# Performance work log

Hardware: AMD Instinct MI355X
Metric: run time of the kernel (lower is better)

Reference implementation:

```python
import jax, jax.numpy as jnp
import numpy as np

N = 100000   # nodes
E = 800000   # edges
F = 64       # num_features == hidden_dim
D = 64       # hidden_dim
L = 3        # num_gc_layers
NG = 512     # num graphs in batch
BN_EPS = 1e-5


def setup_inputs() -> dict:
    key = jax.random.key(0)
    ks = jax.random.split(key, 16)
    s = 0.05
    return {
        "x": jax.random.normal(ks[0], (N, F), jnp.float32),
        "edge_index": jax.random.randint(ks[1], (2, E), 0, N),
        "batch": jnp.sort(jax.random.randint(ks[2], (N,), 0, NG)),
        "W1": jax.random.normal(ks[3], (L, F, D), jnp.float32) * s,
        "b1": jnp.zeros((L, D), jnp.float32),
        "W2": jax.random.normal(ks[4], (L, D, D), jnp.float32) * s,
        "b2": jnp.zeros((L, D), jnp.float32),
        "gin_eps": jnp.zeros((L,), jnp.float32),
        "gin_bias": jnp.zeros((L, D), jnp.float32),
        "bn_gamma": jnp.ones((L, D), jnp.float32),
        "bn_beta": jnp.zeros((L, D), jnp.float32),
        "Wp1": jax.random.normal(ks[5], (L * D, L * D), jnp.float32) * s,
        "bp1": jnp.zeros((L * D,), jnp.float32),
        "Wp2": jax.random.normal(ks[6], (L * D, L * D), jnp.float32) * s,
        "bp2": jnp.zeros((L * D,), jnp.float32),
    }


def reference(x, edge_index, batch, W1, b1, W2, b2, gin_eps, gin_bias,
              bn_gamma, bn_beta, Wp1, bp1, Wp2, bp2):
    row, col = edge_index[0], edge_index[1]
    h = x
    xs = []
    for i in range(L):
        # sparse adj @ h : sum over incoming edges (adj[row, col] = 1)
        agg = jax.ops.segment_sum(h[col], row, num_segments=N)
        z = (1.0 + gin_eps[i]) * h + agg
        # GIN internal MLP: Linear -> ReLU -> Linear -> ReLU
        z = jax.nn.relu(z @ W1[i] + b1[i])
        z = jax.nn.relu(z @ W2[i] + b2[i])
        # conv bias + relu (outer F.relu in Encoder is idempotent)
        z = jax.nn.relu(z + gin_bias[i])
        # BatchNorm1d, training mode: batch stats over nodes, biased variance
        mean = jnp.mean(z, axis=0)
        var = jnp.mean(jnp.square(z - mean), axis=0)
        h = (z - mean) * jax.lax.rsqrt(var + BN_EPS) * bn_gamma[i] + bn_beta[i]
        xs.append(h)
    # per-layer global add pool over graphs, then concat -> [NG, L*D]
    pooled = jnp.concatenate(
        [jax.ops.segment_sum(xi, batch, num_segments=NG) for xi in xs], axis=1)
    # projection head: Linear -> ReLU -> Linear
    y = jax.nn.relu(pooled @ Wp1 + bp1) @ Wp2 + bp2
    return y
```

## Files before the change

kernel.cpp:

```cpp
#include <hip/hip_runtime.h>

#define N_NODES 100000
#define N_EDGES 800000
#define DF 64
#define NGRAPH 512
#define LDIM 192
#define BN_EPS 1e-5
#define NTILES 6250
#define GIN_GRID 782
#define NWT (GIN_GRID * 8)
#define COLS_CAP 2600000
#define NBUCK 782
#define BCAP 2048
#define NBLK 128
#define CHUNK 6250
#define REGION_CAP 6144
#define PROJ_ROWS 8

typedef __attribute__((ext_vector_type(8))) short bf16x8;
typedef __attribute__((ext_vector_type(4))) float f32x4;

__device__ inline short f2bf(float x) {
    union { float f; unsigned u; } v; v.f = x;
    unsigned r = v.u + 0x7fff + ((v.u >> 16) & 1);
    return (short)(r >> 16);
}
__device__ inline float bf2f(unsigned short u) {
    union { unsigned u; float f; } v; v.u = ((unsigned)u) << 16; return v.f;
}
__device__ inline float bflo(unsigned u) {
    union { unsigned x; float f; } v; v.x = u << 16; return v.f;
}
__device__ inline float bfhi(unsigned u) {
    union { unsigned x; float f; } v; v.x = u & 0xffff0000u; return v.f;
}

__global__ __launch_bounds__(256) void x2bf_kernel(
    const float* __restrict__ x, unsigned short* __restrict__ xb)
{
    int i = blockIdx.x * 256 + threadIdx.x;
    const int total = N_NODES * DF / 8;
    if (i >= total) return;
    const float4* src = (const float4*)(x + (size_t)i * 8);
    float4 a = src[0], b = src[1];
    unsigned short u0 = (unsigned short)f2bf(a.x), u1 = (unsigned short)f2bf(a.y);
    unsigned short u2 = (unsigned short)f2bf(a.z), u3 = (unsigned short)f2bf(a.w);
    unsigned short u4 = (unsigned short)f2bf(b.x), u5 = (unsigned short)f2bf(b.y);
    unsigned short u6 = (unsigned short)f2bf(b.z), u7 = (unsigned short)f2bf(b.w);
    uint4 o;
    o.x = (unsigned)u0 | ((unsigned)u1 << 16);
    o.y = (unsigned)u2 | ((unsigned)u3 << 16);
    o.z = (unsigned)u4 | ((unsigned)u5 << 16);
    o.w = (unsigned)u6 | ((unsigned)u7 << 16);
    ((uint4*)xb)[i] = o;
}

__global__ __launch_bounds__(256) void blk_hist_kernel(
    const int* __restrict__ ei, int* __restrict__ hist)
{
    __shared__ int hh[NBUCK];
    int blk = blockIdx.x, tid = threadIdx.x;
    for (int i = tid; i < NBUCK; i += 256) hh[i] = 0;
    __syncthreads();
    int start = blk * CHUNK, end = min(start + CHUNK, N_EDGES);
    for (int e = start + tid; e < end; e += 256)
        atomicAdd(&hh[ei[e] >> 7], 1);
    __syncthreads();
    for (int i = tid; i < NBUCK; i += 256) hist[blk * NBUCK + i] = hh[i];
}

__global__ __launch_bounds__(NBLK) void blk_scan_kernel(
    const int* __restrict__ hist, int* __restrict__ pos, int* __restrict__ cnt)
{
    __shared__ int buf[NBLK];
    int k = blockIdx.x, b = threadIdx.x;
    int v = hist[b * NBUCK + k];
    buf[b] = v;
    __syncthreads();
    for (int o = 1; o < NBLK; o <<= 1) {
        int t = (b >= o) ? buf[b - o] : 0;
        __syncthreads();
        buf[b] += t;
        __syncthreads();
    }
    pos[b * NBUCK + k] = buf[b] - v;
    if (b == NBLK - 1) cnt[k] = buf[b];
}

__global__ __launch_bounds__(256) void place_kernel(
    const int* __restrict__ ei, const int* __restrict__ pos,
    unsigned* __restrict__ bucketData)
{
    __shared__ int cursor[NBUCK];
    int blk = blockIdx.x, tid = threadIdx.x;
    for (int i = tid; i < NBUCK; i += 256) cursor[i] = pos[blk * NBUCK + i];
    __syncthreads();
    int start = blk * CHUNK, end = min(start + CHUNK, N_EDGES);
    for (int e = start + tid; e < end; e += 256) {
        int r = ei[e];
        int c = ei[N_EDGES + e];
        int k = r >> 7;
        int p = atomicAdd(&cursor[k], 1);
        bucketData[(size_t)k * BCAP + p] = ((unsigned)(r & 127) << 17) | (unsigned)c;
    }
}

__global__ __launch_bounds__(256) void bucket_count_kernel(
    const unsigned* __restrict__ bucketData, const int* __restrict__ cnt,
    int* __restrict__ deg, int* __restrict__ bpad)
{
    __shared__ int rc[128];
    __shared__ int wps[16];
    int b = blockIdx.x, tid = threadIdx.x;
    int rowbase = b << 7;
    int nrows = min(128, N_NODES - rowbase);
    int cntb = cnt[b];
    if (tid < 128) rc[tid] = 0;
    __syncthreads();
    for (int e = tid; e < cntb; e += 256)
        atomicAdd(&rc[bucketData[(size_t)b * BCAP + e] >> 17], 1);
    __syncthreads();
    if (tid < nrows) deg[rowbase + tid] = rc[tid];
    if (tid < 16) {
        int m = 0;
        #pragma unroll
        for (int i = 0; i < 8; ++i) m = max(m, rc[tid * 8 + i]);
        wps[tid] = (m + 1) & ~1;
    }
    __syncthreads();
    if (tid == 0) {
        int s = 0;
        #pragma unroll
        for (int pk = 0; pk < 16; ++pk) s += 8 * wps[pk];
        bpad[b] = s;
    }
}

__global__ __launch_bounds__(1024) void bucket_scan_kernel(
    const int* __restrict__ bpad, int* __restrict__ bbase)
{
    __shared__ int buf[1024];
    int tid = threadIdx.x;
    int own = (tid < NBUCK) ? bpad[tid] : 0;
    buf[tid] = own;
    __syncthreads();
    for (int o = 1; o < 1024; o <<= 1) {
        int t = (tid >= o) ? buf[tid - o] : 0;
        __syncthreads();
        buf[tid] += t;
        __syncthreads();
    }
    if (tid < NBUCK) bbase[tid] = buf[tid] - own;
}

__global__ __launch_bounds__(256) void bucket_emit_kernel(
    const unsigned* __restrict__ bucketData, const int* __restrict__ cnt,
    const int* __restrict__ bbase,
    int* __restrict__ colT, int* __restrict__ offT, int* __restrict__ widT)
{
    __shared__ int rc[128], rcur[128];
    __shared__ int wps[16], pstart[16];
    __shared__ int region[REGION_CAP];
    __shared__ int totalS;
    int b = blockIdx.x, tid = threadIdx.x;
    int rowbase = b << 7;
    int nrows = min(128, N_NODES - rowbase);
    int cntb = cnt[b];
    int base = bbase[b];
    if (tid < 128) { rc[tid] = 0; rcur[tid] = 0; }
    __syncthreads();
    for (int e = tid; e < cntb; e += 256)
        atomicAdd(&rc[bucketData[(size_t)b * BCAP + e] >> 17], 1);
    __syncthreads();
    if (tid < 16) {
        int m = 0;
        #pragma unroll
        for (int i = 0; i < 8; ++i) m = max(m, rc[tid * 8 + i]);
        wps[tid] = (m + 1) & ~1;
    }
    __syncthreads();
    if (tid == 0) {
        int run = 0;
        #pragma unroll
        for (int pk = 0; pk < 16; ++pk) { pstart[pk] = run; run += 8 * wps[pk]; }
        totalS = run;
    }
    __syncthreads();
    int total = totalS;
    for (int e = tid; e < cntb; e += 256) {
        unsigned p = bucketData[(size_t)b * BCAP + e];
        int lr = p >> 17;
        int c = p & 0x1FFFF;
        int slot = atomicAdd(&rcur[lr], 1);
        int pk = lr >> 3, g = lr & 7;
        region[pstart[pk] + slot * 8 + g] = c * DF;
    }
    __syncthreads();
    for (int i = tid; i < nrows; i += 256) {
        int pk = i >> 3, g = i & 7;
        int wp = wps[pk];
        int sent = (rowbase + i) * DF;
        for (int slot = rc[i]; slot < wp; ++slot)
            region[pstart[pk] + slot * 8 + g] = sent;
    }
    __syncthreads();
    for (int k = tid; k < total; k += 256) colT[base + k] = region[k];
    if (tid < 16 && tid * 8 < nrows) {
        offT[b * 16 + tid] = base + pstart[tid];
        widT[b * 16 + tid] = wps[tid];
    }
}

__global__ __launch_bounds__(256) void gstart_kernel(
    const int* __restrict__ batch, int* __restrict__ gstart,
    float* __restrict__ idsc, float* __restrict__ idsh)
{
    int g = blockIdx.x * 256 + threadIdx.x;
    if (g < 64) { idsc[g] = 1.0f; idsh[g] = 0.0f; }
    if (g > NGRAPH) return;
    if (g == NGRAPH) { gstart[g] = N_NODES; return; }
    int lo = 0, hi = N_NODES;
    while (lo < hi) {
        int mid = (lo + hi) >> 1;
        if (batch[mid] < g) lo = mid + 1; else hi = mid;
    }
    gstart[g] = lo;
}

__global__ __launch_bounds__(256) void pack_w_kernel(
    const float* __restrict__ W1, const float* __restrict__ W2,
    short* __restrict__ Wpk)
{
    int u = blockIdx.x;
    int layer = u >> 1, gm = u & 1;
    const float* W = (gm ? W2 : W1) + layer * 4096;
    short* dst = Wpk + u * 4096;
    for (int idx = threadIdx.x; idx < 4096; idx += 256) {
        int i = idx & 7;
        int l = (idx >> 3) & 63;
        int rest = idx >> 9;
        int kt = rest & 1, nt = rest >> 1;
        int k = kt * 32 + (l >> 4) * 8 + i;
        int n = nt * 16 + (l & 15);
        dst[idx] = f2bf(W[k * 64 + n]);
    }
}

__global__ __launch_bounds__(512) void gin_layer_kernel(
    const unsigned short* __restrict__ zpb,
    const float* __restrict__ sc_in,
    const float* __restrict__ sh_in,
    const int* __restrict__ offT,
    const int* __restrict__ widT,
    const int* __restrict__ deg,
    const int* __restrict__ colT,
    const int* __restrict__ batch,
    unsigned short* __restrict__ zout,
    float* __restrict__ pooled,
    int lOff,
    const short* __restrict__ Wpk,
    const float* __restrict__ b1,
    const float* __restrict__ b2,
    const float* __restrict__ gin_eps,
    const float* __restrict__ gin_bias,
    float* __restrict__ part_s,
    float* __restrict__ part_q)
{
    __shared__ __align__(16) short Wp1s[4096];
    __shared__ __align__(16) short Wp2s[4096];
    __shared__ __align__(16) short zs[8][16 * 80];

    int tid = threadIdx.x;
    {
        const short4* s1 = (const short4*)Wpk;
        const short4* s2 = (const short4*)(Wpk + 4096);
        short4* d1 = (short4*)Wp1s;
        short4* d2 = (short4*)Wp2s;
        for (int i = tid; i < 1024; i += 512) { d1[i] = s1[i]; d2[i] = s2[i]; }
    }

    int w = tid >> 6, l = tid & 63;
    int lr = l & 15;
    int lk = l >> 4;
    int g8 = l >> 3;
    int j8 = l & 7;
    float epsf = 1.0f + gin_eps[0];
    float b1f[4], b2f[4], gbf[4];
    #pragma unroll
    for (int nt = 0; nt < 4; ++nt) {
        b1f[nt] = b1[nt * 16 + lr];
        b2f[nt] = b2[nt * 16 + lr];
        gbf[nt] = gin_bias[nt * 16 + lr];
    }
    float4 sca = *(const float4*)&sc_in[j8 * 8];
    float4 scb = *(const float4*)&sc_in[j8 * 8 + 4];
    float4 sha = *(const float4*)&sh_in[j8 * 8];
    float4 shb = *(const float4*)&sh_in[j8 * 8 + 4];
    float ssum[4] = {0, 0, 0, 0}, sq[4] = {0, 0, 0, 0};
    short* zw = zs[w];
    __syncthreads();

    int t = blockIdx.x * 8 + w;
    bool active = t < NTILES;
    int n0 = t * 16;
    int g0 = 0;
    bool uni = true;
    int gr[4];

    if (active) {
        g0 = batch[n0];
        int gl = batch[n0 + (l & 15)];
        uni = __all(gl == g0);
        if (!uni) {
            #pragma unroll
            for (int r = 0; r < 4; ++r) gr[r] = batch[n0 + lk * 4 + r];
        }

        #pragma unroll
        for (int half = 0; half < 2; ++half) {
            int p = t * 2 + half;
            int nP0 = p * 8;
            int sP = __builtin_amdgcn_readfirstlane(offT[p]);
            int wP = __builtin_amdgcn_readfirstlane(widT[p]);
            float acc[8];
            #pragma unroll
            for (int i = 0; i < 8; ++i) acc[i] = 0.0f;
            if (wP > 0) {
                int co0 = colT[sP + g8];
                int co1 = colT[sP + 8 + g8];
                uint4 v0 = *(const uint4*)(zpb + co0 + j8 * 8);
                uint4 v1 = *(const uint4*)(zpb + co1 + j8 * 8);
                #pragma unroll 1
                for (int it = 2; it < wP; it += 2) {
                    int cn0 = colT[sP + it * 8 + g8];
                    int cn1 = colT[sP + it * 8 + 8 + g8];
                    uint4 nv0 = *(const uint4*)(zpb + cn0 + j8 * 8);
                    uint4 nv1 = *(const uint4*)(zpb + cn1 + j8 * 8);
                    acc[0] += bflo(v0.x) + bflo(v1.x);
                    acc[1] += bfhi(v0.x) + bfhi(v1.x);
                    acc[2] += bflo(v0.y) + bflo(v1.y);
                    acc[3] += bfhi(v0.y) + bfhi(v1.y);
                    acc[4] += bflo(v0.z) + bflo(v1.z);
                    acc[5] += bfhi(v0.z) + bfhi(v1.z);
                    acc[6] += bflo(v0.w) + bflo(v1.w);
                    acc[7] += bfhi(v0.w) + bfhi(v1.w);
                    v0 = nv0; v1 = nv1;
                }
                acc[0] += bflo(v0.x) + bflo(v1.x);
                acc[1] += bfhi(v0.x) + bfhi(v1.x);
                acc[2] += bflo(v0.y) + bflo(v1.y);
                acc[3] += bfhi(v0.y) + bfhi(v1.y);
                acc[4] += bflo(v0.z) + bflo(v1.z);
                acc[5] += bfhi(v0.z) + bfhi(v1.z);
                acc[6] += bflo(v0.w) + bflo(v1.w);
                acc[7] += bfhi(v0.w) + bfhi(v1.w);
            }
            int node = nP0 + g8;
            int d = deg[node];
            uint4 hv = *(const uint4*)(zpb + node * DF + j8 * 8);
            float hn[8] = { bflo(hv.x), bfhi(hv.x), bflo(hv.y), bfhi(hv.y),
                            bflo(hv.z), bfhi(hv.z), bflo(hv.w), bfhi(hv.w) };
            float np = (float)(wP - d);
            float em = epsf - np;
            float dh = epsf + (float)d;
            float scv[8] = { sca.x, sca.y, sca.z, sca.w, scb.x, scb.y, scb.z, scb.w };
            float shv[8] = { sha.x, sha.y, sha.z, sha.w, shb.x, shb.y, shb.z, shb.w };
            unsigned short us[8];
            #pragma unroll
            for (int i = 0; i < 8; ++i) {
                float zf = scv[i] * (em * hn[i] + acc[i]) + dh * shv[i];
                us[i] = (unsigned short)f2bf(zf);
            }
            uint4 zpk;
            zpk.x = (unsigned)us[0] | ((unsigned)us[1] << 16);
            zpk.y = (unsigned)us[2] | ((unsigned)us[3] << 16);
            zpk.z = (unsigned)us[4] | ((unsigned)us[5] << 16);
            zpk.w = (unsigned)us[6] | ((unsigned)us[7] << 16);
            *(uint4*)&zw[(half * 8 + g8) * 80 + j8 * 8] = zpk;
        }

        {
            bf16x8 a0 = *(const bf16x8*)&zw[lr * 80 + lk * 8];
            bf16x8 a1 = *(const bf16x8*)&zw[lr * 80 + 32 + lk * 8];
            #pragma unroll
            for (int nt = 0; nt < 4; ++nt) {
                f32x4 acc = {0.f, 0.f, 0.f, 0.f};
                bf16x8 bb0 = *(const bf16x8*)&Wp1s[((nt * 2 + 0) * 64 + l) * 8];
                bf16x8 bb1 = *(const bf16x8*)&Wp1s[((nt * 2 + 1) * 64 + l) * 8];
                acc = __builtin_amdgcn_mfma_f32_16x16x32_bf16(a0, bb0, acc, 0, 0, 0);
                acc = __builtin_amdgcn_mfma_f32_16x16x32_bf16(a1, bb1, acc, 0, 0, 0);
                #pragma unroll
                for (int r = 0; r < 4; ++r) {
                    float v = fmaxf(acc[r] + b1f[nt], 0.0f);
                    zw[(lk * 4 + r) * 80 + nt * 16 + lr] = f2bf(v);
                }
            }
        }

        {
            bf16x8 a0 = *(const bf16x8*)&zw[lr * 80 + lk * 8];
            bf16x8 a1 = *(const bf16x8*)&zw[lr * 80 + 32 + lk * 8];
            #pragma unroll
            for (int nt = 0; nt < 4; ++nt) {
                f32x4 acc = {0.f, 0.f, 0.f, 0.f};
                bf16x8 bb0 = *(const bf16x8*)&Wp2s[((nt * 2 + 0) * 64 + l) * 8];
                bf16x8 bb1 = *(const bf16x8*)&Wp2s[((nt * 2 + 1) * 64 + l) * 8];
                acc = __builtin_amdgcn_mfma_f32_16x16x32_bf16(a0, bb0, acc, 0, 0, 0);
                acc = __builtin_amdgcn_mfma_f32_16x16x32_bf16(a1, bb1, acc, 0, 0, 0);
                #pragma unroll
                for (int r = 0; r < 4; ++r) {
                    float v = fmaxf(fmaxf(acc[r] + b2f[nt], 0.0f) + gbf[nt], 0.0f);
                    unsigned short vb = (unsigned short)f2bf(v);
                    zout[(n0 + lk * 4 + r) * DF + nt * 16 + lr] = vb;
                    float vr = bf2f(vb);
                    ssum[nt] += vr;
                    sq[nt] += vr * vr;
                    if (!uni)
                        unsafeAtomicAdd(&pooled[gr[r] * LDIM + lOff + nt * 16 + lr], vr);
                }
            }
        }
    }

    float svv[4];
    #pragma unroll
    for (int nt = 0; nt < 4; ++nt) {
        float sv = ssum[nt], qv = sq[nt];
        sv += __shfl_xor(sv, 16, 64); sv += __shfl_xor(sv, 32, 64);
        qv += __shfl_xor(qv, 16, 64); qv += __shfl_xor(qv, 32, 64);
        svv[nt] = sv;
        if (l < 16) {
            part_s[(nt * 16 + l) * NWT + t] = sv;
            part_q[(nt * 16 + l) * NWT + t] = qv;
        }
    }
    if (active && uni && l < 16) {
        #pragma unroll
        for (int nt = 0; nt < 4; ++nt)
            unsafeAtomicAdd(&pooled[g0 * LDIM + lOff + nt * 16 + l], svv[nt]);
    }
}

__global__ __launch_bounds__(256) void stat_reduce_kernel(
    const float* __restrict__ part_s, const float* __restrict__ part_q,
    const float* __restrict__ gamma, const float* __restrict__ beta,
    float* __restrict__ scale, float* __restrict__ shift)
{
    __shared__ double rs[4], rq[4];
    int f = blockIdx.x, tid = threadIdx.x;
    double s = 0.0, q = 0.0;
    for (int j = tid; j < NWT; j += 256) {
        s += (double)part_s[f * NWT + j];
        q += (double)part_q[f * NWT + j];
    }
    for (int o = 32; o > 0; o >>= 1) {
        s += __shfl_down(s, o, 64);
        q += __shfl_down(q, o, 64);
    }
    if ((tid & 63) == 0) { rs[tid >> 6] = s; rq[tid >> 6] = q; }
    __syncthreads();
    if (tid == 0) {
        double st = rs[0] + rs[1] + rs[2] + rs[3];
        double qt = rq[0] + rq[1] + rq[2] + rq[3];
        double mean = st / N_NODES;
        double var = qt / N_NODES - mean * mean;
        double inv = (double)gamma[f] / sqrt(var + BN_EPS);
        scale[f] = (float)inv;
        shift[f] = (float)((double)beta[f] - mean * inv);
    }
}

__global__ __launch_bounds__(192) void proj_fused_kernel(
    const float* __restrict__ praw,
    const float* __restrict__ scale3, const float* __restrict__ shift3,
    const int* __restrict__ gstart,
    const float* __restrict__ Wp1, const float* __restrict__ bp1,
    const float* __restrict__ Wp2, const float* __restrict__ bp2,
    float* __restrict__ out)
{
    __shared__ float rowS[PROJ_ROWS][LDIM];
    __shared__ float hid[PROJ_ROWS][LDIM];
    int r0 = blockIdx.x * PROJ_ROWS;
    int c = threadIdx.x;
    float scc = scale3[c], shc = shift3[c];
    #pragma unroll
    for (int r = 0; r < PROJ_ROWS; ++r) {
        int g = r0 + r;
        float cntg = (float)(gstart[g + 1] - gstart[g]);
        rowS[r][c] = scc * praw[g * LDIM + c] + cntg * shc;
    }
    __syncthreads();

    float acc[PROJ_ROWS];
    float bv = bp1[c];
    #pragma unroll
    for (int r = 0; r < PROJ_ROWS; ++r) acc[r] = bv;
    for (int k = 0; k < LDIM; ++k) {
        float wv = Wp1[k * LDIM + c];
        #pragma unroll
        for (int r = 0; r < PROJ_ROWS; ++r) acc[r] += rowS[r][k] * wv;
    }
    #pragma unroll
    for (int r = 0; r < PROJ_ROWS; ++r) hid[r][c] = fmaxf(acc[r], 0.0f);
    __syncthreads();

    float bv2 = bp2[c];
    #pragma unroll
    for (int r = 0; r < PROJ_ROWS; ++r) acc[r] = bv2;
    for (int k = 0; k < LDIM; ++k) {
        float wv = Wp2[k * LDIM + c];
        #pragma unroll
        for (int r = 0; r < PROJ_ROWS; ++r) acc[r] += hid[r][k] * wv;
    }
    #pragma unroll
    for (int r = 0; r < PROJ_ROWS; ++r)
        out[(r0 + r) * LDIM + c] = acc[r];
}

extern "C" void kernel_launch(void* const* d_in, const int* in_sizes, int n_in,
                              void* d_out, int out_size, void* d_ws, size_t ws_size,
                              hipStream_t stream)
{
    const float* x        = (const float*)d_in[0];
    const int*   ei       = (const int*)d_in[1];
    const int*   batch    = (const int*)d_in[2];
    const float* W1       = (const float*)d_in[3];
    const float* b1       = (const float*)d_in[4];
    const float* W2       = (const float*)d_in[5];
    const float* b2       = (const float*)d_in[6];
    const float* gin_eps  = (const float*)d_in[7];
    const float* gin_bias = (const float*)d_in[8];
    const float* gamma    = (const float*)d_in[9];
    const float* beta     = (const float*)d_in[10];
    const float* Wp1      = (const float*)d_in[11];
    const float* bp1      = (const float*)d_in[12];
    const float* Wp2      = (const float*)d_in[13];
    const float* bp2      = (const float*)d_in[14];
    float* out = (float*)d_out;

    unsigned short* xb    = (unsigned short*)d_ws;
    unsigned short* zbufA = xb + (size_t)N_NODES * DF;
    unsigned short* zbufB = zbufA + (size_t)N_NODES * DF;
    float* pooled = (float*)(zbufB + (size_t)N_NODES * DF);
    float* scale3 = pooled + (size_t)NGRAPH * LDIM;
    float* shift3 = scale3 + LDIM;
    float* idsc = shift3 + LDIM;
    float* idsh = idsc + 64;
    float* part_s = idsh + 64;
    float* part_q = part_s + (size_t)64 * NWT;
    int* gstart = (int*)(part_q + (size_t)64 * NWT);
    int* deg  = gstart + NGRAPH + 1;
    int* offT = deg + N_NODES;
    int* widT = offT + 16 * NBUCK;
    int* colT = widT + 16 * NBUCK;
    int* hist = colT + COLS_CAP;
    int* pos  = hist + NBLK * NBUCK;
    int* cnt  = pos + NBLK * NBUCK;
    int* bpad = cnt + NBUCK;
    int* bbase = bpad + NBUCK;
    unsigned* bucketData = (unsigned*)(bbase + NBUCK);
    short* Wpk = (short*)(bucketData + (size_t)NBUCK * BCAP);

    hipMemsetAsync(pooled, 0, (size_t)NGRAPH * LDIM * sizeof(float), stream);
    x2bf_kernel<<<(N_NODES * DF / 8 + 255) / 256, 256, 0, stream>>>(x, xb);
    blk_hist_kernel<<<NBLK, 256, 0, stream>>>(ei, hist);
    blk_scan_kernel<<<NBUCK, NBLK, 0, stream>>>(hist, pos, cnt);
    place_kernel<<<NBLK, 256, 0, stream>>>(ei, pos, bucketData);
    bucket_count_kernel<<<NBUCK, 256, 0, stream>>>(bucketData, cnt, deg, bpad);
    bucket_scan_kernel<<<1, 1024, 0, stream>>>(bpad, bbase);
    bucket_emit_kernel<<<NBUCK, 256, 0, stream>>>(bucketData, cnt, bbase,
                                                  colT, offT, widT);
    gstart_kernel<<<3, 256, 0, stream>>>(batch, gstart, idsc, idsh);
    pack_w_kernel<<<6, 256, 0, stream>>>(W1, W2, Wpk);

    unsigned short* zbuf[2] = {zbufA, zbufB};
    const unsigned short* zprev = xb;
    const float* sc_in = idsc;
    const float* sh_in = idsh;
    for (int l = 0; l < 3; ++l) {
        unsigned short* zcur = zbuf[l & 1];
        gin_layer_kernel<<<GIN_GRID, 512, 0, stream>>>(
            zprev, sc_in, sh_in, offT, widT, deg, colT, batch, zcur,
            pooled, l * 64,
            Wpk + (size_t)l * 8192,
            b1 + l * 64, b2 + l * 64, gin_eps + l, gin_bias + l * 64,
            part_s, part_q);

        stat_reduce_kernel<<<64, 256, 0, stream>>>(
            part_s, part_q, gamma + l * 64, beta + l * 64,
            scale3 + l * 64, shift3 + l * 64);

        zprev = zcur;
        sc_in = scale3 + l * 64;
        sh_in = shift3 + l * 64;
    }

    proj_fused_kernel<<<NGRAPH / PROJ_ROWS, LDIM, 0, stream>>>(
        pooled, scale3, shift3, gstart, Wp1, bp1, Wp2, bp2, out);
}
```

Before: 240.7 us.

## Renumber nodes by in-degree within each graph to balance padded CSR groups

Adds a degree histogram and a per-graph counting sort that permute node IDs so nodes with similar in-degree sit next to each other, while each node stays inside its graph's contiguous range so pooling by batch still holds. The features and edge endpoints are remapped through the permutation. The aim is to cut padding in the 8-row groups whose width is set by their widest row, which wastes gather work in the GIN layers. It costs three extra small kernels, an extra memset and indirect gathers in the preprocessing steps. It also relies on per-graph sums and batch-norm statistics being order-independent so the output stays correct.

Measured after the change: 291.1 us. 1.21x slower.

```diff
diff --git a/kernel.cpp b/kernel.cpp
--- a/kernel.cpp
+++ b/kernel.cpp
@@ -35,13 +35,64 @@
     union { unsigned x; float f; } v; v.x = u & 0xffff0000u; return v.f;
 }
 
+__global__ __launch_bounds__(256) void deg_hist_kernel(
+    const int* __restrict__ ei, int* __restrict__ degP)
+{
+    int e = blockIdx.x * 256 + threadIdx.x;
+    if (e < N_EDGES) atomicAdd(&degP[ei[e]], 1);
+}
+
+__global__ __launch_bounds__(256) void gstart_kernel(
+    const int* __restrict__ batch, int* __restrict__ gstart,
+    float* __restrict__ idsc, float* __restrict__ idsh)
+{
+    int g = blockIdx.x * 256 + threadIdx.x;
+    if (g < 64) { idsc[g] = 1.0f; idsh[g] = 0.0f; }
+    if (g > NGRAPH) return;
+    if (g == NGRAPH) { gstart[g] = N_NODES; return; }
+    int lo = 0, hi = N_NODES;
+    while (lo < hi) {
+        int mid = (lo + hi) >> 1;
+        if (batch[mid] < g) lo = mid + 1; else hi = mid;
+    }
+    gstart[g] = lo;
+}
+
+__global__ __launch_bounds__(256) void sort_kernel(
+    const int* __restrict__ gstart, const int* __restrict__ degP,
+    int* __restrict__ perm, int* __restrict__ invp)
+{
+    __shared__ int bins[64], cur[64];
+    int g = blockIdx.x, tid = threadIdx.x;
+    int s0 = gstart[g], cnt = gstart[g + 1] - s0;
+    if (tid < 64) bins[tid] = 0;
+    __syncthreads();
+    for (int i = tid; i < cnt; i += 256)
+        atomicAdd(&bins[min(degP[s0 + i], 63)], 1);
+    __syncthreads();
+    if (tid == 0) {
+        int run = 0;
+        for (int d = 0; d < 64; ++d) { int v = bins[d]; cur[d] = run; run += v; }
+    }
+    __syncthreads();
+    for (int i = tid; i < cnt; i += 256) {
+        int d = min(degP[s0 + i], 63);
+        int slot = atomicAdd(&cur[d], 1);
+        perm[s0 + slot] = s0 + i;
+        invp[s0 + i] = s0 + slot;
+    }
+}
+
 __global__ __launch_bounds__(256) void x2bf_kernel(
-    const float* __restrict__ x, unsigned short* __restrict__ xb)
+    const float* __restrict__ x, const int* __restrict__ perm,
+    unsigned short* __restrict__ xb)
 {
     int i = blockIdx.x * 256 + threadIdx.x;
     const int total = N_NODES * DF / 8;
     if (i >= total) return;
-    const float4* src = (const float4*)(x + (size_t)i * 8);
+    int node = i >> 3, j = i & 7;
+    int phys = perm[node];
+    const float4* src = (const float4*)(x + (size_t)phys * DF + j * 8);
     float4 a = src[0], b = src[1];
     unsigned short u0 = (unsigned short)f2bf(a.x), u1 = (unsigned short)f2bf(a.y);
     unsigned short u2 = (unsigned short)f2bf(a.z), u3 = (unsigned short)f2bf(a.w);
@@ -56,7 +107,8 @@
 }
 
 __global__ __launch_bounds__(256) void blk_hist_kernel(
-    const int* __restrict__ ei, int* __restrict__ hist)
+    const int* __restrict__ ei, const int* __restrict__ invp,
+    int* __restrict__ hist)
 {
     __shared__ int hh[NBUCK];
     int blk = blockIdx.x, tid = threadIdx.x;
@@ -64,7 +116,7 @@
     __syncthreads();
     int start = blk * CHUNK, end = min(start + CHUNK, N_EDGES);
     for (int e = start + tid; e < end; e += 256)
-        atomicAdd(&hh[ei[e] >> 7], 1);
+        atomicAdd(&hh[invp[ei[e]] >> 7], 1);
     __syncthreads();
     for (int i = tid; i < NBUCK; i += 256) hist[blk * NBUCK + i] = hh[i];
 }
@@ -88,8 +140,8 @@
 }
 
 __global__ __launch_bounds__(256) void place_kernel(
-    const int* __restrict__ ei, const int* __restrict__ pos,
-    unsigned* __restrict__ bucketData)
+    const int* __restrict__ ei, const int* __restrict__ invp,
+    const int* __restrict__ pos, unsigned* __restrict__ bucketData)
 {
     __shared__ int cursor[NBUCK];
     int blk = blockIdx.x, tid = threadIdx.x;
@@ -97,11 +149,11 @@
     __syncthreads();
     int start = blk * CHUNK, end = min(start + CHUNK, N_EDGES);
     for (int e = start + tid; e < end; e += 256) {
-        int r = ei[e];
-        int c = ei[N_EDGES + e];
-        int k = r >> 7;
+        int pr = invp[ei[e]];
+        int pc = invp[ei[N_EDGES + e]];
+        int k = pr >> 7;
         int p = atomicAdd(&cursor[k], 1);
-        bucketData[(size_t)k * BCAP + p] = ((unsigned)(r & 127) << 17) | (unsigned)c;
+        bucketData[(size_t)k * BCAP + p] = ((unsigned)(pr & 127) << 17) | (unsigned)pc;
     }
 }
 
@@ -209,22 +261,6 @@
         offT[b * 16 + tid] = base + pstart[tid];
         widT[b * 16 + tid] = wps[tid];
     }
-}
-
-__global__ __launch_bounds__(256) void gstart_kernel(
-    const int* __restrict__ batch, int* __restrict__ gstart,
-    float* __restrict__ idsc, float* __restrict__ idsh)
-{
-    int g = blockIdx.x * 256 + threadIdx.x;
-    if (g < 64) { idsc[g] = 1.0f; idsh[g] = 0.0f; }
-    if (g > NGRAPH) return;
-    if (g == NGRAPH) { gstart[g] = N_NODES; return; }
-    int lo = 0, hi = N_NODES;
-    while (lo < hi) {
-        int mid = (lo + hi) >> 1;
-        if (batch[mid] < g) lo = mid + 1; else hi = mid;
-    }
-    gstart[g] = lo;
 }
 
 __global__ __launch_bounds__(256) void pack_w_kernel(
@@ -550,7 +586,10 @@
     float* part_q = part_s + (size_t)64 * NWT;
     int* gstart = (int*)(part_q + (size_t)64 * NWT);
     int* deg  = gstart + NGRAPH + 1;
-    int* offT = deg + N_NODES;
+    int* degP = deg + N_NODES;
+    int* perm = degP + N_NODES;
+    int* invp = perm + N_NODES;
+    int* offT = invp + N_NODES;
     int* widT = offT + 16 * NBUCK;
     int* colT = widT + 16 * NBUCK;
     int* hist = colT + COLS_CAP;
@@ -562,15 +601,18 @@
     short* Wpk = (short*)(bucketData + (size_t)NBUCK * BCAP);
 
     hipMemsetAsync(pooled, 0, (size_t)NGRAPH * LDIM * sizeof(float), stream);
-    x2bf_kernel<<<(N_NODES * DF / 8 + 255) / 256, 256, 0, stream>>>(x, xb);
-    blk_hist_kernel<<<NBLK, 256, 0, stream>>>(ei, hist);
+    hipMemsetAsync(degP, 0, N_NODES * sizeof(int), stream);
+    deg_hist_kernel<<<(N_EDGES + 255) / 256, 256, 0, stream>>>(ei, degP);
+    gstart_kernel<<<3, 256, 0, stream>>>(batch, gstart, idsc, idsh);
+    sort_kernel<<<NGRAPH, 256, 0, stream>>>(gstart, degP, perm, invp);
+    x2bf_kernel<<<(N_NODES * DF / 8 + 255) / 256, 256, 0, stream>>>(x, perm, xb);
+    blk_hist_kernel<<<NBLK, 256, 0, stream>>>(ei, invp, hist);
     blk_scan_kernel<<<NBUCK, NBLK, 0, stream>>>(hist, pos, cnt);
-    place_kernel<<<NBLK, 256, 0, stream>>>(ei, pos, bucketData);
+    place_kernel<<<NBLK, 256, 0, stream>>>(ei, invp, pos, bucketData);
     bucket_count_kernel<<<NBUCK, 256, 0, stream>>>(bucketData, cnt, deg, bpad);
     bucket_scan_kernel<<<1, 1024, 0, stream>>>(bpad, bbase);
     bucket_emit_kernel<<<NBUCK, 256, 0, stream>>>(bucketData, cnt, bbase,
                                                   colT, offT, widT);
-    gstart_kernel<<<3, 256, 0, stream>>>(batch, gstart, idsc, idsh);
     pack_w_kernel<<<6, 256, 0, stream>>>(W1, W2, Wpk);
 
     unsigned short* zbuf[2] = {zbufA, zbufB};
```
